# Performance work log

Hardware: AMD Instinct MI355X
Metric: run time of the kernel (lower is better)

The kernel has to match this reference:

```python
import jax, jax.numpy as jnp
import numpy as np

D_MODEL = 2048
NUM_EXPERTS = 64
TOP_K = 2


def setup_inputs() -> dict:
    key = jax.random.key(0)
    kx, kw, kb = jax.random.split(key, 3)
    x = jax.random.normal(kx, (4, 4096, D_MODEL), dtype=jnp.float32)
    # nn.Linear(d_model, num_experts): weight [num_experts, d_model], bias [num_experts]
    bound = 1.0 / np.sqrt(D_MODEL)
    W = jax.random.uniform(kw, (NUM_EXPERTS, D_MODEL), minval=-bound, maxval=bound, dtype=jnp.float32)
    b = jax.random.uniform(kb, (NUM_EXPERTS,), minval=-bound, maxval=bound, dtype=jnp.float32)
    return {"x": x, "W": W, "b": b}


def reference(x, W, b):
    # Eval mode: no noise injection (self.training is False).
    logits = jnp.einsum('bsd,ed->bse', x, W) + b          # [B, S, E]
    raw_weights = jax.nn.softmax(logits, axis=-1)          # [B, S, E]
    top_k_weights, top_k_indices = jax.lax.top_k(raw_weights, TOP_K)  # [B, S, K]
    normalized = top_k_weights / jnp.sum(top_k_weights, axis=-1, keepdims=True)
    return normalized, top_k_indices
```

## Files before the change

kernel.cpp:

```cpp
#include <hip/hip_runtime.h>
#include <math.h>

#define DM 2048
#define NEXP 64
#define NTOK 16384
#define NSLICE 8
#define KSL (DM / NSLICE)
#define KC 32
#define NCH (KSL / KC)
#define MB 128
#define NBLK1 ((NTOK / MB) * NSLICE)
#define WFRAG_BYTES (64 * 12 * 1024)
#define PART_BYTES (NSLICE * NTOK * NEXP * 4)

typedef __attribute__((ext_vector_type(8))) short short8;
typedef __attribute__((ext_vector_type(4))) float f32x4;

__device__ __forceinline__ void async16(void* lds, const void* g) {
  __builtin_amdgcn_global_load_lds(
      (const __attribute__((address_space(1))) unsigned int*)g,
      (__attribute__((address_space(3))) unsigned int*)lds, 16, 0, 0);
}

__device__ __forceinline__ void split3t(float f, unsigned short& h,
                                        unsigned short& m, unsigned short& l) {
  unsigned u = __float_as_uint(f);
  h = (unsigned short)(u >> 16);
  float f1 = f - __uint_as_float(u & 0xFFFF0000u);
  unsigned u1 = __float_as_uint(f1);
  m = (unsigned short)(u1 >> 16);
  float f2 = f1 - __uint_as_float(u1 & 0xFFFF0000u);
  l = (unsigned short)(__float_as_uint(f2) >> 16);
}

__device__ __forceinline__ void split8(const f32x4& a0, const f32x4& a1,
                                       short8& h, short8& m, short8& l) {
  float v[8] = {a0[0], a0[1], a0[2], a0[3], a1[0], a1[1], a1[2], a1[3]};
#pragma unroll
  for (int j = 0; j < 8; ++j) {
    unsigned short hh, mm, ll;
    split3t(v[j], hh, mm, ll);
    h[j] = (short)hh; m[j] = (short)mm; l[j] = (short)ll;
  }
}

__global__ void convw_kernel(const float* __restrict__ W,
                             unsigned short* __restrict__ wfrag) {
  const int kg = blockIdx.x;
  const int lane = threadIdx.x & 63;
  const int nt = threadIdx.x >> 6;
  const int e = nt * 16 + (lane & 15);
  const int kpos = kg * 32 + (lane >> 4) * 8;
  const f32x4* wp = (const f32x4*)(W + (size_t)e * DM + kpos);
  f32x4 w0 = wp[0], w1 = wp[1];
  short8 h, m, l;
  split8(w0, w1, h, m, l);
  size_t base = ((size_t)(kg * 12 + nt) * 64 + lane) * 8;
  *(short8*)(wfrag + base) = h;
  *(short8*)(wfrag + base + (size_t)4 * 64 * 8) = m;
  *(short8*)(wfrag + base + (size_t)8 * 64 * 8) = l;
}

__global__ __launch_bounds__(256, 4)
void router_gemm(const float* __restrict__ x,
                 const unsigned short* __restrict__ wfrag,
                 float* __restrict__ part) {
  const int lane = threadIdx.x & 63;
  const int wv = threadIdx.x >> 6;
  const int col = lane & 15;
  const int quad = lane >> 4;
  const int tg = blockIdx.x & ((NTOK / MB) - 1);
  const int s = blockIdx.x >> 7;
  const int tok0 = tg * MB;

  __shared__ __align__(16) float xs[MB][KC];
  __shared__ __align__(16) unsigned short bs[12][64][8];

  f32x4 acc[2][4];
#pragma unroll
  for (int mt = 0; mt < 2; ++mt)
#pragma unroll
    for (int nt = 0; nt < 4; ++nt) acc[mt][nt] = (f32x4){0.f, 0.f, 0.f, 0.f};

  for (int c = 0; c < NCH; ++c) {
    const int kc = s * KSL + c * KC;
    const int kg = s * NCH + c;

#pragma unroll
    for (int i = 0; i < 4; ++i) {
      const int r = wv * 32 + i * 8;
      const int tr = r + (lane >> 3);
      const int unit = (lane & 7) ^ ((lane >> 3) & 7);
      async16(&xs[r][0],
              x + (size_t)(tok0 + tr) * DM + kc + unit * 4);
    }
#pragma unroll
    for (int q = 0; q < 3; ++q) {
      const int m = wv * 3 + q;
      async16(&bs[m][0][0],
              wfrag + ((size_t)kg * 12 + m) * 512 + (size_t)lane * 8);
    }
    __syncthreads();

    short8 ah[2], am[2], al[2];
#pragma unroll
    for (int mt = 0; mt < 2; ++mt) {
      const int row = wv * 32 + mt * 16 + col;
      const int u0 = (quad * 2) ^ (row & 7);
      const int u1 = (quad * 2 + 1) ^ (row & 7);
      f32x4 a0 = *(const f32x4*)&xs[row][u0 * 4];
      f32x4 a1 = *(const f32x4*)&xs[row][u1 * 4];
      split8(a0, a1, ah[mt], am[mt], al[mt]);
    }

#pragma unroll
    for (int nt = 0; nt < 4; ++nt) {
      short8 bh = *(const short8*)&bs[nt][lane][0];
      short8 bm = *(const short8*)&bs[4 + nt][lane][0];
      short8 bl = *(const short8*)&bs[8 + nt][lane][0];
#pragma unroll
      for (int mt = 0; mt < 2; ++mt) {
        f32x4 cc = acc[mt][nt];
        cc = __builtin_amdgcn_mfma_f32_16x16x32_bf16(ah[mt], bh, cc, 0, 0, 0);
        cc = __builtin_amdgcn_mfma_f32_16x16x32_bf16(ah[mt], bm, cc, 0, 0, 0);
        cc = __builtin_amdgcn_mfma_f32_16x16x32_bf16(am[mt], bh, cc, 0, 0, 0);
        cc = __builtin_amdgcn_mfma_f32_16x16x32_bf16(ah[mt], bl, cc, 0, 0, 0);
        cc = __builtin_amdgcn_mfma_f32_16x16x32_bf16(al[mt], bh, cc, 0, 0, 0);
        cc = __builtin_amdgcn_mfma_f32_16x16x32_bf16(am[mt], bm, cc, 0, 0, 0);
        acc[mt][nt] = cc;
      }
    }
    __syncthreads();
  }

#pragma unroll
  for (int mt = 0; mt < 2; ++mt)
#pragma unroll
    for (int nt = 0; nt < 4; ++nt)
#pragma unroll
      for (int r = 0; r < 4; ++r) {
        const int token = tok0 + wv * 32 + mt * 16 + quad * 4 + r;
        const int e = nt * 16 + col;
        part[((size_t)s * NTOK + token) * NEXP + e] = acc[mt][nt][r];
      }
}

__global__ __launch_bounds__(256, 8)
void router_reduce(const float* __restrict__ part,
                   const float* __restrict__ bias, float* __restrict__ out) {
  const int lane = threadIdx.x & 63;
  const int wv = threadIdx.x >> 6;
  const float bl = bias[lane];
  const int t0 = blockIdx.x * 8 + wv * 2;
#pragma unroll
  for (int tt = 0; tt < 2; ++tt) {
    const int t = t0 + tt;
    float p[NSLICE];
#pragma unroll
    for (int sl = 0; sl < NSLICE; ++sl)
      p[sl] = part[((size_t)sl * NTOK + t) * NEXP + lane];
    float v1 = bl;
#pragma unroll
    for (int sl = 0; sl < NSLICE; ++sl) v1 += p[sl];
    int i1 = lane;
    float v2 = -INFINITY;
    int i2 = NEXP;
#pragma unroll
    for (int off = 32; off > 0; off >>= 1) {
      float ov1 = __shfl_xor(v1, off, 64);
      int   oi1 = __shfl_xor(i1, off, 64);
      float ov2 = __shfl_xor(v2, off, 64);
      int   oi2 = __shfl_xor(i2, off, 64);
      bool afirst = (v1 > ov1) || (v1 == ov1 && i1 < oi1);
      float w1v = afirst ? v1 : ov1;  int w1i = afirst ? i1 : oi1;
      float c1v = afirst ? v2 : ov2;  int c1i = afirst ? i2 : oi2;
      float c2v = afirst ? ov1 : v1;  int c2i = afirst ? oi1 : i1;
      bool sfirst = (c1v > c2v) || (c1v == c2v && c1i < c2i);
      v1 = w1v; i1 = w1i;
      v2 = sfirst ? c1v : c2v;
      i2 = sfirst ? c1i : c2i;
    }
    if (lane == 0) {
      const float ex = expf(v2 - v1);
      const float den = 1.f + ex;
      *(float2*)(out + 2 * t) = make_float2(1.f / den, ex / den);
      *(float2*)(out + 2 * NTOK + 2 * t) = make_float2((float)i1, (float)i2);
    }
  }
}

__global__ __launch_bounds__(512, 2)
void router_fb(const float* __restrict__ x, const float* __restrict__ W,
               const float* __restrict__ bias, float* __restrict__ out) {
  const int lane = threadIdx.x & 63;
  const int wv = threadIdx.x >> 6;
  const int col = lane & 15;
  const int quad = lane >> 4;
  const int tok0 = blockIdx.x * 32;
  const int k0 = wv * 256;

  __shared__ float part[8][32][68];

  f32x4 acc[2][4];
#pragma unroll
  for (int ms = 0; ms < 2; ++ms)
#pragma unroll
    for (int nt = 0; nt < 4; ++nt) acc[ms][nt] = (f32x4){0.f, 0.f, 0.f, 0.f};

  for (int ks = 0; ks < 8; ++ks) {
    const int k = k0 + ks * 32 + quad * 8;
    short8 ah[2], am2[2], al2[2];
#pragma unroll
    for (int ms = 0; ms < 2; ++ms) {
      const f32x4* ap = (const f32x4*)(x + (size_t)(tok0 + ms * 16 + col) * DM + k);
      f32x4 a0 = ap[0], a1 = ap[1];
      split8(a0, a1, ah[ms], am2[ms], al2[ms]);
    }
#pragma unroll
    for (int nt = 0; nt < 4; ++nt) {
      short8 bh, bm, bl;
      const f32x4* wp = (const f32x4*)(W + (size_t)(nt * 16 + col) * DM + k);
      f32x4 w0 = wp[0], w1 = wp[1];
      split8(w0, w1, bh, bm, bl);
#pragma unroll
      for (int ms = 0; ms < 2; ++ms) {
        f32x4 cc = acc[ms][nt];
        cc = __builtin_amdgcn_mfma_f32_16x16x32_bf16(ah[ms], bh, cc, 0, 0, 0);
        cc = __builtin_amdgcn_mfma_f32_16x16x32_bf16(ah[ms], bm, cc, 0, 0, 0);
        cc = __builtin_amdgcn_mfma_f32_16x16x32_bf16(am2[ms], bh, cc, 0, 0, 0);
        cc = __builtin_amdgcn_mfma_f32_16x16x32_bf16(ah[ms], bl, cc, 0, 0, 0);
        cc = __builtin_amdgcn_mfma_f32_16x16x32_bf16(al2[ms], bh, cc, 0, 0, 0);
        cc = __builtin_amdgcn_mfma_f32_16x16x32_bf16(am2[ms], bm, cc, 0, 0, 0);
        acc[ms][nt] = cc;
      }
    }
  }
#pragma unroll
  for (int ms = 0; ms < 2; ++ms)
#pragma unroll
    for (int nt = 0; nt < 4; ++nt)
#pragma unroll
      for (int r = 0; r < 4; ++r)
        part[wv][ms * 16 + quad * 4 + r][nt * 16 + col] = acc[ms][nt][r];
  __syncthreads();
  const float bl_ = bias[lane];
#pragma unroll
  for (int ti = 0; ti < 4; ++ti) {
    const int t = wv * 4 + ti;
    float v1 = bl_;
#pragma unroll
    for (int p = 0; p < 8; ++p) v1 += part[p][t][lane];
    int i1 = lane;
    float v2 = -INFINITY;
    int i2 = NEXP;
#pragma unroll
    for (int off = 32; off > 0; off >>= 1) {
      float ov1 = __shfl_xor(v1, off, 64);
      int   oi1 = __shfl_xor(i1, off, 64);
      float ov2 = __shfl_xor(v2, off, 64);
      int   oi2 = __shfl_xor(i2, off, 64);
      bool afirst = (v1 > ov1) || (v1 == ov1 && i1 < oi1);
      float w1v = afirst ? v1 : ov1;  int w1i = afirst ? i1 : oi1;
      float c1v = afirst ? v2 : ov2;  int c1i = afirst ? i2 : oi2;
      float c2v = afirst ? ov1 : v1;  int c2i = afirst ? oi1 : i1;
      bool sfirst = (c1v > c2v) || (c1v == c2v && c1i < c2i);
      v1 = w1v; i1 = w1i;
      v2 = sfirst ? c1v : c2v;
      i2 = sfirst ? c1i : c2i;
    }
    if (lane == 0) {
      const float ex = expf(v2 - v1);
      const float den = 1.f + ex;
      const int token = tok0 + t;
      *(float2*)(out + 2 * token) = make_float2(1.f / den, ex / den);
      *(float2*)(out + 2 * NTOK + 2 * token) =
          make_float2((float)i1, (float)i2);
    }
  }
}

extern "C" void kernel_launch(void* const* d_in, const int* in_sizes, int n_in,
                              void* d_out, int out_size, void* d_ws, size_t ws_size,
                              hipStream_t stream) {
  const float* x = (const float*)d_in[0];
  const float* W = (const float*)d_in[1];
  const float* b = (const float*)d_in[2];
  float* out = (float*)d_out;

  const size_t need = (size_t)WFRAG_BYTES + (size_t)PART_BYTES;
  if (ws_size >= need) {
    unsigned short* wfrag = (unsigned short*)d_ws;
    float* part = (float*)((char*)d_ws + WFRAG_BYTES);
    hipLaunchKernelGGL(convw_kernel, dim3(64), dim3(256), 0, stream, W, wfrag);
    hipLaunchKernelGGL(router_gemm, dim3(NBLK1), dim3(256), 0, stream,
                       x, wfrag, part);
    hipLaunchKernelGGL(router_reduce, dim3(NTOK / 8), dim3(256), 0, stream,
                       part, b, out);
  } else {
    hipLaunchKernelGGL(router_fb, dim3(NTOK / 32), dim3(512), 0, stream,
                       x, W, b, out);
  }
}
```

Before: 217.3 us.

## Double-buffer router GEMM LDS loads and halve split-K slices and token tile

The router GEMM gains double-buffered LDS staging. The next K chunk's x and weight fragments are issued asynchronously before computing the current chunk, using vmcnt-based barriers in place of full syncthreads. The token tile per block drops from 128 to 64 (one 16-row M tile per wave) and the split-K slice count from 8 to 4. The block index now maps slices to the low bits so that blocks sharing a token group run close together. This aims to hide global-load latency and cut partial-sum traffic in the reduce kernel, at the cost of more LDS per block and less MFMA reuse of the B fragments per wave.

```diff
diff --git a/kernel.cpp b/kernel.cpp
--- a/kernel.cpp
+++ b/kernel.cpp
@@ -4,13 +4,14 @@
 #define DM 2048
 #define NEXP 64
 #define NTOK 16384
-#define NSLICE 8
+#define NSLICE 4
 #define KSL (DM / NSLICE)
 #define KC 32
 #define NCH (KSL / KC)
-#define MB 128
+#define MB 64
 #define NBLK1 ((NTOK / MB) * NSLICE)
-#define WFRAG_BYTES (64 * 12 * 1024)
+#define NKG (DM / KC)
+#define WFRAG_BYTES (NKG * 12 * 1024)
 #define PART_BYTES (NSLICE * NTOK * NEXP * 4)
 
 typedef __attribute__((ext_vector_type(8))) short short8;
@@ -21,6 +22,13 @@
       (const __attribute__((address_space(1))) unsigned int*)g,
       (__attribute__((address_space(3))) unsigned int*)lds, 16, 0, 0);
 }
+
+#define PIPE_BARRIER_KEEP5() \
+  asm volatile("s_waitcnt vmcnt(5)\n\ts_barrier" ::: "memory")
+#define PIPE_BARRIER_DRAIN() \
+  asm volatile("s_waitcnt vmcnt(0)\n\ts_barrier" ::: "memory")
+#define COMPUTE_DONE_BARRIER() \
+  asm volatile("s_waitcnt lgkmcnt(0)\n\ts_barrier" ::: "memory")
 
 __device__ __forceinline__ void split3t(float f, unsigned short& h,
                                         unsigned short& m, unsigned short& l) {
@@ -69,80 +77,76 @@
   const int wv = threadIdx.x >> 6;
   const int col = lane & 15;
   const int quad = lane >> 4;
-  const int tg = blockIdx.x & ((NTOK / MB) - 1);
-  const int s = blockIdx.x >> 7;
+  const int tg = blockIdx.x >> 2;
+  const int s = blockIdx.x & 3;
   const int tok0 = tg * MB;
 
-  __shared__ __align__(16) float xs[MB][KC];
-  __shared__ __align__(16) unsigned short bs[12][64][8];
-
-  f32x4 acc[2][4];
-#pragma unroll
-  for (int mt = 0; mt < 2; ++mt)
-#pragma unroll
-    for (int nt = 0; nt < 4; ++nt) acc[mt][nt] = (f32x4){0.f, 0.f, 0.f, 0.f};
+  __shared__ __align__(16) float xs[2][MB][KC];
+  __shared__ __align__(16) unsigned short bs[2][12][64][8];
+
+  const int xrow_in = lane >> 3;
+  const int xunit = (lane & 7) ^ (xrow_in & 7);
+  const float* xsrc0 =
+      x + (size_t)(tok0 + wv * 16 + xrow_in) * DM + s * KSL + xunit * 4;
+  const unsigned short* bsrc0 =
+      wfrag + ((size_t)(s * NCH) * 12 + wv * 3) * 512 + (size_t)lane * 8;
+
+  f32x4 acc[4];
+#pragma unroll
+  for (int nt = 0; nt < 4; ++nt) acc[nt] = (f32x4){0.f, 0.f, 0.f, 0.f};
+
+  auto stage = [&](int buf, int c) {
+#pragma unroll
+    for (int i = 0; i < 2; ++i)
+      async16(&xs[buf][wv * 16 + i * 8][0], xsrc0 + i * 8 * DM + c * KC);
+#pragma unroll
+    for (int q = 0; q < 3; ++q)
+      async16(&bs[buf][wv * 3 + q][0][0], bsrc0 + ((size_t)c * 12 + q) * 512);
+  };
+
+  stage(0, 0);
 
   for (int c = 0; c < NCH; ++c) {
-    const int kc = s * KSL + c * KC;
-    const int kg = s * NCH + c;
-
-#pragma unroll
-    for (int i = 0; i < 4; ++i) {
-      const int r = wv * 32 + i * 8;
-      const int tr = r + (lane >> 3);
-      const int unit = (lane & 7) ^ ((lane >> 3) & 7);
-      async16(&xs[r][0],
-              x + (size_t)(tok0 + tr) * DM + kc + unit * 4);
-    }
-#pragma unroll
-    for (int q = 0; q < 3; ++q) {
-      const int m = wv * 3 + q;
-      async16(&bs[m][0][0],
-              wfrag + ((size_t)kg * 12 + m) * 512 + (size_t)lane * 8);
-    }
-    __syncthreads();
-
-    short8 ah[2], am[2], al[2];
-#pragma unroll
-    for (int mt = 0; mt < 2; ++mt) {
-      const int row = wv * 32 + mt * 16 + col;
-      const int u0 = (quad * 2) ^ (row & 7);
-      const int u1 = (quad * 2 + 1) ^ (row & 7);
-      f32x4 a0 = *(const f32x4*)&xs[row][u0 * 4];
-      f32x4 a1 = *(const f32x4*)&xs[row][u1 * 4];
-      split8(a0, a1, ah[mt], am[mt], al[mt]);
-    }
+    const int cur = c & 1;
+    if (c + 1 < NCH) {
+      stage(cur ^ 1, c + 1);
+      PIPE_BARRIER_KEEP5();
+    } else {
+      PIPE_BARRIER_DRAIN();
+    }
+
+    const int row = wv * 16 + col;
+    const int u0 = (quad * 2) ^ (col & 7);
+    const int u1 = (quad * 2 + 1) ^ (col & 7);
+    f32x4 a0 = *(const f32x4*)&xs[cur][row][u0 * 4];
+    f32x4 a1 = *(const f32x4*)&xs[cur][row][u1 * 4];
+    short8 ah, am, al;
+    split8(a0, a1, ah, am, al);
 
 #pragma unroll
     for (int nt = 0; nt < 4; ++nt) {
-      short8 bh = *(const short8*)&bs[nt][lane][0];
-      short8 bm = *(const short8*)&bs[4 + nt][lane][0];
-      short8 bl = *(const short8*)&bs[8 + nt][lane][0];
-#pragma unroll
-      for (int mt = 0; mt < 2; ++mt) {
-        f32x4 cc = acc[mt][nt];
-        cc = __builtin_amdgcn_mfma_f32_16x16x32_bf16(ah[mt], bh, cc, 0, 0, 0);
-        cc = __builtin_amdgcn_mfma_f32_16x16x32_bf16(ah[mt], bm, cc, 0, 0, 0);
-        cc = __builtin_amdgcn_mfma_f32_16x16x32_bf16(am[mt], bh, cc, 0, 0, 0);
-        cc = __builtin_amdgcn_mfma_f32_16x16x32_bf16(ah[mt], bl, cc, 0, 0, 0);
-        cc = __builtin_amdgcn_mfma_f32_16x16x32_bf16(al[mt], bh, cc, 0, 0, 0);
-        cc = __builtin_amdgcn_mfma_f32_16x16x32_bf16(am[mt], bm, cc, 0, 0, 0);
-        acc[mt][nt] = cc;
-      }
-    }
-    __syncthreads();
-  }
-
-#pragma unroll
-  for (int mt = 0; mt < 2; ++mt)
-#pragma unroll
-    for (int nt = 0; nt < 4; ++nt)
-#pragma unroll
-      for (int r = 0; r < 4; ++r) {
-        const int token = tok0 + wv * 32 + mt * 16 + quad * 4 + r;
-        const int e = nt * 16 + col;
-        part[((size_t)s * NTOK + token) * NEXP + e] = acc[mt][nt][r];
-      }
+      short8 bh = *(const short8*)&bs[cur][nt][lane][0];
+      short8 bm = *(const short8*)&bs[cur][4 + nt][lane][0];
+      short8 bl = *(const short8*)&bs[cur][8 + nt][lane][0];
+      f32x4 cc = acc[nt];
+      cc = __builtin_amdgcn_mfma_f32_16x16x32_bf16(ah, bh, cc, 0, 0, 0);
+      cc = __builtin_amdgcn_mfma_f32_16x16x32_bf16(ah, bm, cc, 0, 0, 0);
+      cc = __builtin_amdgcn_mfma_f32_16x16x32_bf16(am, bh, cc, 0, 0, 0);
+      cc = __builtin_amdgcn_mfma_f32_16x16x32_bf16(ah, bl, cc, 0, 0, 0);
+      cc = __builtin_amdgcn_mfma_f32_16x16x32_bf16(al, bh, cc, 0, 0, 0);
+      cc = __builtin_amdgcn_mfma_f32_16x16x32_bf16(am, bm, cc, 0, 0, 0);
+      acc[nt] = cc;
+    }
+    COMPUTE_DONE_BARRIER();
+  }
+
+#pragma unroll
+  for (int nt = 0; nt < 4; ++nt)
+#pragma unroll
+    for (int r = 0; r < 4; ++r) {
+      const int token = tok0 + wv * 16 + quad * 4 + r;
+      part[((size_t)s * NTOK + token) * NEXP + nt * 16 + col] = acc[nt][r];
+    }
 }
 
 __global__ __launch_bounds__(256, 8)
@@ -155,13 +159,10 @@
 #pragma unroll
   for (int tt = 0; tt < 2; ++tt) {
     const int t = t0 + tt;
-    float p[NSLICE];
+    float v1 = bl;
 #pragma unroll
     for (int sl = 0; sl < NSLICE; ++sl)
-      p[sl] = part[((size_t)sl * NTOK + t) * NEXP + lane];
-    float v1 = bl;
-#pragma unroll
-    for (int sl = 0; sl < NSLICE; ++sl) v1 += p[sl];
+      v1 += part[((size_t)sl * NTOK + t) * NEXP + lane];
     int i1 = lane;
     float v2 = -INFINITY;
     int i2 = NEXP;
@@ -291,7 +292,7 @@
   if (ws_size >= need) {
     unsigned short* wfrag = (unsigned short*)d_ws;
     float* part = (float*)((char*)d_ws + WFRAG_BYTES);
-    hipLaunchKernelGGL(convw_kernel, dim3(64), dim3(256), 0, stream, W, wfrag);
+    hipLaunchKernelGGL(convw_kernel, dim3(NKG), dim3(256), 0, stream, W, wfrag);
     hipLaunchKernelGGL(router_gemm, dim3(NBLK1), dim3(256), 0, stream,
                        x, wfrag, part);
     hipLaunchKernelGGL(router_reduce, dim3(NTOK / 8), dim3(256), 0, stream,
```

New measurement: 207.7 us. -4.4%, faster.
